# Kernel optimization log

Hardware: AMD Instinct MI355X
Metric: run time of the kernel (lower is better)

Reference implementation:

```python
import jax, jax.numpy as jnp
import numpy as np

N_NODES = 30000
N_EDGES = 600000
N_BATCH = 8
VFRAMES = 3
EPS = 1e-20


def rbf_func(D, num_rbf=16):
    # RBF over [0, 20] with num_rbf centers, matching torch rbf_func
    mu = jnp.linspace(0.0, 20.0, num_rbf).astype(D.dtype)
    sigma = 20.0 / num_rbf
    return jnp.exp(-(((D[..., None] - mu) / sigma) ** 2))


def decouple(U):
    # split vector into unit direction (zeroed when tiny) + RBF of its norm -> last dim 3+16
    sq = jnp.sum(U * U, axis=-1, keepdims=True)
    norm = jnp.sqrt(sq + 1e-12)  # tiny eps for grad safety; fwd diff negligible
    direct = jnp.where(norm < 1e-4, 0.0, U / (norm + 1e-6))
    return jnp.concatenate([direct, rbf_func(norm[..., 0])], axis=-1)


def int_embedding(d, num_embeddings):
    freq = jnp.exp(jnp.arange(0, num_embeddings, 2, dtype=jnp.float32) * (-np.log(10000.0) / num_embeddings))
    ang = d.astype(jnp.float32)[:, None] * freq[None, :]
    return jnp.concatenate([jnp.cos(ang), jnp.sin(ang)], axis=-1)


def make_frames(n_xyz, ca_xyz, c_xyz):
    # openfold Rigid.make_transform_from_reference -> R [N,3,3], t = CA [N,3]
    n = n_xyz - ca_xyz
    c = c_xyz - ca_xyz
    cx, cy, cz = c[:, 0], c[:, 1], c[:, 2]
    z = jnp.zeros_like(cx)
    o = jnp.ones_like(cx)
    nrm = jnp.sqrt(EPS + cx ** 2 + cy ** 2)
    s1, c1 = -cy / nrm, cx / nrm
    R1 = jnp.stack([c1, -s1, z, s1, c1, z, z, z, o], -1).reshape(-1, 3, 3)
    nrm2 = jnp.sqrt(EPS + cx ** 2 + cy ** 2 + cz ** 2)
    s2 = cz / nrm2
    c2 = jnp.sqrt(cx ** 2 + cy ** 2) / nrm2
    R2 = jnp.stack([c2, z, s2, z, o, z, -s2, z, c2], -1).reshape(-1, 3, 3)
    Rc = jnp.matmul(R2, R1)
    nrot = jnp.einsum('nij,nj->ni', Rc, n)
    ny, nz2 = nrot[:, 1], nrot[:, 2]
    nrm3 = jnp.sqrt(EPS + ny ** 2 + nz2 ** 2)
    sn, cn = -nz2 / nrm3, ny / nrm3
    Rn = jnp.stack([o, z, z, z, cn, -sn, z, sn, cn], -1).reshape(-1, 3, 3)
    R = jnp.swapaxes(jnp.matmul(Rn, Rc), -1, -2)
    return R, ca_xyz


def geo_features(X, node_idx, edge_idx, batch_id, num_batches, virtual_frame_num):
    N = X.shape[0]
    E = edge_idx.shape[1]
    B = num_batches          # static python int
    K = virtual_frame_num    # static python int
    src, dst = edge_idx[0], edge_idx[1]
    R, t = make_frames(X[:, 0], X[:, 1], X[:, 2])
    # relative transform T_ts = T[dst]^-1 . T[src]
    Rts = jnp.einsum('eji,ejk->eik', R[dst], R[src])            # [E,3,3]
    tts = jnp.einsum('eji,ej->ei', R[dst], t[src] - t[dst])     # [E,3]
    # node feats: consecutive-atom diffs, zeroed at each chain start, rotated into local frame
    flat = X.reshape(-1, 3)
    d = jnp.concatenate([jnp.zeros((1, 3), X.dtype), flat[1:] - flat[:-1]], 0).reshape(N, 4, 3)
    counts = jax.ops.segment_sum(jnp.ones_like(batch_id), batch_id, num_segments=B)
    shift = jnp.roll(jnp.cumsum(counts).at[-1].set(0), 1)       # chain start offsets
    d = d.at[shift].set(0.0)
    dX_loc = jnp.einsum('nji,naj->nai', R, d)                   # R^T @ d
    V = jnp.nan_to_num(decouple(dX_loc).reshape(N, -1))         # [N,76]
    # edge feats: both endpoints' atoms in src local frame
    pts = jnp.concatenate([X[src], X[dst]], axis=1)             # [E,8,3]
    loc = jnp.einsum('eji,eaj->eai', R[src], pts - t[src][:, None])
    diffE = decouple(loc).reshape(E, -1)                        # [E,152]
    pos = int_embedding((src - dst), 16)                        # [E,16]
    E_quant = jnp.swapaxes(Rts, -1, -2).reshape(E, 9)           # inverse rel-rot flattened
    E_trans = decouple(tts).reshape(E, -1)                      # [E,19]
    b = (node_idx[src] - node_idx[dst]).astype(X.dtype)
    E_bias = decouple(b[:, None, None]).reshape(E, -1)          # [E,17]
    Efeat = jnp.concatenate([diffE, E_quant, E_trans, pos, E_bias], axis=-1)  # [E,213]
    # virtual (global) frames: K virtual nodes per protein, identity frames (geo_frame=False)
    g_src = jnp.concatenate([N + batch_id + k * B for k in range(K)])   # [K*N]
    g_dst = jnp.tile(jnp.arange(N, dtype=batch_id.dtype), K)
    eidx_g = jnp.concatenate([jnp.stack([g_src, g_dst]), jnp.stack([g_dst, g_src])], axis=1)
    bid_g = jnp.tile(jnp.arange(B, dtype=batch_id.dtype), K)            # [K*B]
    V_g = int_embedding(jnp.repeat(jnp.arange(K), B), V.shape[-1]).astype(X.dtype)
    E_g = jnp.zeros((2 * K * N, Efeat.shape[-1]), Efeat.dtype)
    eyeKB = jnp.broadcast_to(jnp.eye(3, dtype=X.dtype), (K * B, 3, 3))
    V_out = jnp.concatenate([V, V_g], 0)
    E_out = jnp.concatenate([Efeat, E_g], 0)
    T_rot = jnp.concatenate([R, eyeKB], 0)
    T_trans = jnp.concatenate([t, jnp.zeros((K * B, 3), X.dtype)], 0)
    Tts_rot = jnp.concatenate([Rts, jnp.broadcast_to(jnp.eye(3, dtype=X.dtype), (2 * K * N, 3, 3))], 0)
    Tts_trans = jnp.concatenate([tts, jnp.zeros((2 * K * N, 3), X.dtype)], 0)
    batch_out = jnp.concatenate([batch_id, bid_g])
    eidx_out = jnp.concatenate([edge_idx, eidx_g], axis=1)
    return V_out, E_out, T_rot, T_trans, Tts_rot, Tts_trans, batch_out, eidx_out


def setup_inputs():
    key = jax.random.key(0)
    k1, k2 = jax.random.split(key)
    X = jax.random.normal(k1, (N_NODES, 4, 3), dtype=jnp.float32) * 4.0
    edge_idx = jax.random.randint(k2, (2, N_EDGES), 0, N_NODES)
    per = N_NODES // N_BATCH
    batch_id = jnp.repeat(jnp.arange(N_BATCH), per)   # sorted, contiguous batches
    node_idx = jnp.tile(jnp.arange(per), N_BATCH)     # residue index within each chain
    chain_encoding = batch_id % 8
    return {"X": X, "node_idx": node_idx, "edge_idx": edge_idx, "batch_id": batch_id,
            "chain_encoding": chain_encoding, "num_batches": N_BATCH, "virtual_frame_num": VFRAMES}


def reference(X, node_idx, edge_idx, batch_id, chain_encoding, num_batches, virtual_frame_num):
    V, Eo, T_rot, T_trans, Tts_rot, Tts_trans, batch_out, eidx_out = geo_features(
        X, node_idx, edge_idx, batch_id, num_batches, virtual_frame_num)
    K, B = virtual_frame_num, num_batches
    chain_out = jnp.concatenate([chain_encoding,
                                 jnp.ones((K * B,), chain_encoding.dtype) + 1000])
    return (V, Eo, T_rot, T_trans, Tts_rot, Tts_trans, batch_out, eidx_out, chain_out)
```

## Files before the change

kernel.cpp:

```cpp
#include <hip/hip_runtime.h>

typedef unsigned int u32;
typedef float f32x4 __attribute__((ext_vector_type(4)));

#define N_NODES 30000
#define N_EDGES 600000
#define NBATCH  8
#define KVF     3
#define PER_B   3750
#define NV      30024
#define EV      780000

#define O_V      0ULL
#define O_E      2281824ULL
#define O_TROT   168421824ULL
#define O_TTRANS 168692040ULL
#define O_TTSROT 168782112ULL
#define O_TTSTR  175802112ULL
#define O_BATCH  178142112ULL
#define O_EIDX   178172136ULL
#define O_CHAIN  179732136ULL

#define TOTAL_BLOCKS 12500
#define NODE_BLOCKS  118
#define FILL_THREADS 769792ULL
#define F_VE   9585000ULL
#define F_ROT  (F_VE + 405000ULL)
#define F_TR   (F_ROT + 135000ULL)
#define F_END  (F_TR + 390000ULL)

__device__ __forceinline__ float2 fast_sincos(float ang) {
    double rev = (double)ang * 0.15915494309189535;
    rev -= rint(rev);
    float r = (float)rev;
    float2 sc;
    sc.x = __builtin_amdgcn_sinf(r);
    sc.y = __builtin_amdgcn_cosf(r);
    return sc;
}

__device__ __forceinline__ void decouple_store(float u0, float u1, float u2, float* dst) {
    float sq   = u0 * u0 + u1 * u1 + u2 * u2;
    float norm = sqrtf(sq + 1e-12f);
    float inv  = (norm < 1e-4f) ? 0.f : (1.f / (norm + 1e-6f));
    dst[0] = u0 * inv;
    dst[1] = u1 * inv;
    dst[2] = u2 * inv;
#pragma unroll
    for (int k = 0; k < 16; ++k) {
        float mu = 1.3333333333333333f * (float)k;
        float z  = (norm - mu) * 0.8f;
        dst[3 + k] = __expf(-z * z);
    }
}

__device__ __forceinline__ void make_frame(float4 x0, float4 x1, float4 x2,
                                           float M[9], float& t0, float& t1, float& t2) {
    float cax = x0.w, cay = x1.x, caz = x1.y;
    float nx = x0.x - cax, ny = x0.y - cay, nz = x0.z - caz;
    float cx = x1.z - cax, cy = x1.w - cay, cz = x2.x - caz;
    float h2   = cx * cx + cy * cy;
    float nrm  = sqrtf(1e-20f + h2);
    float s1 = -cy / nrm, c1 = cx / nrm;
    float nrm2 = sqrtf(1e-20f + h2 + cz * cz);
    float s2 = cz / nrm2, c2 = sqrtf(h2) / nrm2;
    float Rc00 = c2 * c1, Rc01 = -c2 * s1, Rc02 = s2;
    float Rc10 = s1,      Rc11 = c1;
    float Rc20 = -s2 * c1, Rc21 = s2 * s1, Rc22 = c2;
    float nr1 = Rc10 * nx + Rc11 * ny;
    float nr2 = Rc20 * nx + Rc21 * ny + Rc22 * nz;
    float nrm3 = sqrtf(1e-20f + nr1 * nr1 + nr2 * nr2);
    float sn = -nr2 / nrm3, cn = nr1 / nrm3;
    M[0] = Rc00;                   M[1] = Rc01;                   M[2] = Rc02;
    M[3] = cn * Rc10 - sn * Rc20;  M[4] = cn * Rc11 - sn * Rc21;  M[5] = -sn * Rc22;
    M[6] = sn * Rc10 + cn * Rc20;  M[7] = sn * Rc11 + cn * Rc21;  M[8] = cn * Rc22;
    t0 = cax; t1 = cay; t2 = caz;
}

__global__ __launch_bounds__(256) void mega_kernel(
        const float* __restrict__ X, const int* __restrict__ eidx,
        const int* __restrict__ node_idx, const int* __restrict__ batch_id,
        const int* __restrict__ chain, float* __restrict__ out) {
    __shared__ __align__(16) float sE[64 * 213];
    __shared__ __align__(16) float sRot[64 * 9];
    __shared__ __align__(16) float sTr[64 * 3];

    int bid = blockIdx.x;
    int tid = threadIdx.x;

    if ((bid & 3) == 3) {
        int oblk = bid >> 2;
        if (oblk < NODE_BLOCKS) {
            int i = oblk * 256 + tid;
            if (i >= NV) return;
            if (i < N_NODES) {
                const float4* xv = (const float4*)(X + (size_t)i * 12);
                float4 x0 = xv[0], x1 = xv[1], x2 = xv[2];
                float M[9], cax, cay, caz;
                make_frame(x0, x1, x2, M, cax, cay, caz);
                float* tr = out + O_TROT + (size_t)i * 9;
                tr[0] = M[0]; tr[1] = M[3]; tr[2] = M[6];
                tr[3] = M[1]; tr[4] = M[4]; tr[5] = M[7];
                tr[6] = M[2]; tr[7] = M[5]; tr[8] = M[8];
                float* tt = out + O_TTRANS + (size_t)i * 3;
                tt[0] = cax; tt[1] = cay; tt[2] = caz;
                const float* xi = X + (size_t)i * 12;
                float* vp = out + O_V + (size_t)i * 76;
                bool zero_d = (i % PER_B) == 0;
#pragma unroll
                for (int a = 0; a < 4; ++a) {
                    float d0, d1, d2;
                    if (zero_d) {
                        d0 = d1 = d2 = 0.f;
                    } else {
                        const float* pc = xi + a * 3;
                        d0 = pc[0] - pc[-3]; d1 = pc[1] - pc[-2]; d2 = pc[2] - pc[-1];
                    }
                    float u0 = M[0] * d0 + M[1] * d1 + M[2] * d2;
                    float u1 = M[3] * d0 + M[4] * d1 + M[5] * d2;
                    float u2 = M[6] * d0 + M[7] * d1 + M[8] * d2;
                    decouple_store(u0, u1, u2, vp + a * 19);
                }
                out[O_BATCH + i] = (float)batch_id[i];
                out[O_CHAIN + i] = (float)chain[i];
            } else {
                int r = i - N_NODES;
                float kv = (float)(r >> 3);
                float* vp = out + O_V + (size_t)i * 76;
#pragma unroll
                for (int j = 0; j < 38; ++j) {
                    float freq = __expf((float)(2 * j) * (-9.210340371976184f / 76.f));
                    float2 sc  = fast_sincos(kv * freq);
                    vp[j]      = sc.y;
                    vp[38 + j] = sc.x;
                }
                float* tr = out + O_TROT + (size_t)i * 9;
#pragma unroll
                for (int j = 0; j < 9; ++j) tr[j] = (j == 0 || j == 4 || j == 8) ? 1.f : 0.f;
                float* tt = out + O_TTRANS + (size_t)i * 3;
                tt[0] = 0.f; tt[1] = 0.f; tt[2] = 0.f;
                out[O_BATCH + i] = (float)(r & 7);
                out[O_CHAIN + i] = 1001.f;
            }
            return;
        }
        f32x4* oE   = (f32x4*)(out + O_E + 600000ULL * 213ULL);
        f32x4* oRot = (f32x4*)(out + O_TTSROT + 5400000ULL);
        f32x4* oTr  = (f32x4*)(out + O_TTSTR + 1800000ULL);
        f32x4* oEi  = (f32x4*)(out + O_EIDX);
        f32x4 zero; zero.x = zero.y = zero.z = zero.w = 0.f;
        for (size_t f = (size_t)(oblk - NODE_BLOCKS) * 256 + tid; f < F_END; f += FILL_THREADS) {
            if (f < F_VE) {
                __builtin_nontemporal_store(zero, oE + f);
            } else if (f < F_ROT) {
                size_t f2 = f - F_VE;
                u32 a = (u32)((f2 * 4ULL) % 9ULL);
                f32x4 w;
#pragma unroll
                for (int l = 0; l < 4; ++l) {
                    w[l] = (a == 0u || a == 4u || a == 8u) ? 1.f : 0.f;
                    a = (a == 8u) ? 0u : a + 1u;
                }
                __builtin_nontemporal_store(w, oRot + f2);
            } else if (f < F_TR) {
                __builtin_nontemporal_store(zero, oTr + (f - F_ROT));
            } else {
                size_t f4 = f - F_TR;
                int i0 = (int)(f4 * 4);
                f32x4 w;
#pragma unroll
                for (int l = 0; l < 4; ++l) {
                    int i = i0 + l;
                    int row = (i >= EV) ? 1 : 0;
                    int col = i - row * EV;
                    float v;
                    if (col < N_EDGES) {
                        v = (float)eidx[row * N_EDGES + col];
                    } else {
                        int j    = col - N_EDGES;
                        int half = j / 90000;
                        int jj   = j - half * 90000;
                        int k    = jj / N_NODES;
                        int node = jj - k * N_NODES;
                        v = (row == half) ? (float)(N_NODES + batch_id[node] + k * NBATCH)
                                          : (float)node;
                    }
                    w[l] = v;
                }
                __builtin_nontemporal_store(w, oEi + f4);
            }
        }
        return;
    }

    int eblk = (bid >> 2) * 3 + (bid & 3);
    int el   = tid & 63;
    int part = tid >> 6;
    int e = eblk * 64 + el;
    int src = eidx[e];
    int dst = eidx[N_EDGES + e];
    float* se = sE + el * 213;

    if (part <= 1) {
        const float4* xs = (const float4*)(X + (size_t)src * 12);
        float4 s0 = xs[0], s1 = xs[1], s2 = xs[2];
        float4 p0 = s0, p1 = s1, p2 = s2;
        if (part == 1) {
            const float4* xd = (const float4*)(X + (size_t)dst * 12);
            p0 = xd[0]; p1 = xd[1]; p2 = xd[2];
        }
        float M[9], ts0, ts1, ts2;
        make_frame(s0, s1, s2, M, ts0, ts1, ts2);
        float px[4] = { p0.x, p0.w, p1.z, p2.y };
        float py[4] = { p0.y, p1.x, p1.w, p2.z };
        float pz[4] = { p0.z, p1.y, p2.x, p2.w };
        float* base = se + (part == 0 ? 0 : 76);
#pragma unroll
        for (int a = 0; a < 4; ++a) {
            float q0 = px[a] - ts0, q1 = py[a] - ts1, q2 = pz[a] - ts2;
            float u0 = M[0] * q0 + M[1] * q1 + M[2] * q2;
            float u1 = M[3] * q0 + M[4] * q1 + M[5] * q2;
            float u2 = M[6] * q0 + M[7] * q1 + M[8] * q2;
            decouple_store(u0, u1, u2, base + a * 19);
        }
    } else if (part == 2) {
        const float4* xs = (const float4*)(X + (size_t)src * 12);
        const float4* xd = (const float4*)(X + (size_t)dst * 12);
        float4 s0 = xs[0], s1 = xs[1], s2 = xs[2];
        float4 d0 = xd[0], d1 = xd[1], d2 = xd[2];
        float Ms[9], ts0, ts1, ts2;
        float Md[9], td0, td1, td2;
        make_frame(s0, s1, s2, Ms, ts0, ts1, ts2);
        make_frame(d0, d1, d2, Md, td0, td1, td2);
        float* sr = sRot + el * 9;
#pragma unroll
        for (int ii = 0; ii < 3; ++ii) {
#pragma unroll
            for (int k = 0; k < 3; ++k) {
                float q = Md[3 * ii] * Ms[3 * k] + Md[3 * ii + 1] * Ms[3 * k + 1]
                        + Md[3 * ii + 2] * Ms[3 * k + 2];
                sr[ii * 3 + k] = q;
                se[152 + k * 3 + ii] = q;
            }
        }
        float dt0 = ts0 - td0, dt1 = ts1 - td1, dt2 = ts2 - td2;
        float t0 = Md[0] * dt0 + Md[1] * dt1 + Md[2] * dt2;
        float t1 = Md[3] * dt0 + Md[4] * dt1 + Md[5] * dt2;
        float t2 = Md[6] * dt0 + Md[7] * dt1 + Md[8] * dt2;
        float* st = sTr + el * 3;
        st[0] = t0; st[1] = t1; st[2] = t2;
        decouple_store(t0, t1, t2, se + 161);
    } else {
        float dd = (float)(src - dst);
#pragma unroll
        for (int j = 0; j < 8; ++j) {
            float freq = __expf((float)(2 * j) * (-9.210340371976184f / 16.f));
            float ang  = dd * freq;
            float2 sc  = fast_sincos(ang);
            se[180 + j] = sc.y;
            se[188 + j] = sc.x;
        }
        float b    = (float)(node_idx[src] - node_idx[dst]);
        float norm = sqrtf(b * b + 1e-12f);
        se[196] = (norm < 1e-4f) ? 0.f : (b / (norm + 1e-6f));
#pragma unroll
        for (int k = 0; k < 16; ++k) {
            float z = (norm - 1.3333333333333333f * (float)k) * 0.8f;
            se[197 + k] = __expf(-z * z);
        }
    }
    __syncthreads();
    const f32x4* s4 = (const f32x4*)sE;
    f32x4* dE = (f32x4*)(out + O_E) + (size_t)eblk * 3408;
    for (int i2 = tid; i2 < 3408; i2 += 256)
        __builtin_nontemporal_store(s4[i2], dE + i2);
    if (tid < 144)
        __builtin_nontemporal_store(((const f32x4*)sRot)[tid],
                                    (f32x4*)(out + O_TTSROT) + (size_t)eblk * 144 + tid);
    if (tid < 48)
        __builtin_nontemporal_store(((const f32x4*)sTr)[tid],
                                    (f32x4*)(out + O_TTSTR) + (size_t)eblk * 48 + tid);
}

extern "C" void kernel_launch(void* const* d_in, const int* in_sizes, int n_in,
                              void* d_out, int out_size, void* d_ws, size_t ws_size,
                              hipStream_t stream) {
    const float* X        = (const float*)d_in[0];
    const int* node_idx   = (const int*)d_in[1];
    const int* eidx       = (const int*)d_in[2];
    const int* batch_id   = (const int*)d_in[3];
    const int* chain      = (const int*)d_in[4];
    float* out = (float*)d_out;
    (void)d_ws; (void)ws_size;

    mega_kernel<<<TOTAL_BLOCKS, 256, 0, stream>>>(X, eidx, node_idx, batch_id, chain, out);
}
```

Baseline: 715.7 us.

## Halve edges per block and split edge work across seven 32-lane parts

Each edge block now handles 32 edges instead of 64. The per-edge work is spread over seven 32-thread parts instead of four 64-thread parts: atom projections are split two per thread, and the sinusoidal and RBF features get separate parts. This gives more blocks, less shared memory per block and better thread utilisation, aimed at reducing per-thread latency and raising occupancy. The interleave of node/fill blocks changes from 1-in-4 to 1-in-7, and the source frame is recomputed in more threads (wave 7 of 8 idle).

```diff
diff --git a/kernel.cpp b/kernel.cpp
--- a/kernel.cpp
+++ b/kernel.cpp
@@ -21,7 +21,7 @@
 #define O_EIDX   178172136ULL
 #define O_CHAIN  179732136ULL
 
-#define TOTAL_BLOCKS 12500
+#define TOTAL_BLOCKS 21875
 #define NODE_BLOCKS  118
 #define FILL_THREADS 769792ULL
 #define F_VE   9585000ULL
@@ -81,15 +81,16 @@
         const float* __restrict__ X, const int* __restrict__ eidx,
         const int* __restrict__ node_idx, const int* __restrict__ batch_id,
         const int* __restrict__ chain, float* __restrict__ out) {
-    __shared__ __align__(16) float sE[64 * 213];
-    __shared__ __align__(16) float sRot[64 * 9];
-    __shared__ __align__(16) float sTr[64 * 3];
+    __shared__ __align__(16) float sE[32 * 213];
+    __shared__ __align__(16) float sRot[32 * 9];
+    __shared__ __align__(16) float sTr[32 * 3];
 
     int bid = blockIdx.x;
     int tid = threadIdx.x;
-
-    if ((bid & 3) == 3) {
-        int oblk = bid >> 2;
+    int sel = bid % 7;
+
+    if (sel == 6) {
+        int oblk = bid / 7;
         if (oblk < NODE_BLOCKS) {
             int i = oblk * 256 + tid;
             if (i >= NV) return;
@@ -193,37 +194,48 @@
         return;
     }
 
-    int eblk = (bid >> 2) * 3 + (bid & 3);
-    int el   = tid & 63;
-    int part = tid >> 6;
-    int e = eblk * 64 + el;
+    int eblk = (bid / 7) * 6 + sel;
+    int el   = tid & 31;
+    int part = tid >> 5;
+    int e = eblk * 32 + el;
     int src = eidx[e];
     int dst = eidx[N_EDGES + e];
     float* se = sE + el * 213;
 
-    if (part <= 1) {
+    if (part < 4) {
         const float4* xs = (const float4*)(X + (size_t)src * 12);
         float4 s0 = xs[0], s1 = xs[1], s2 = xs[2];
         float4 p0 = s0, p1 = s1, p2 = s2;
-        if (part == 1) {
+        if (part >= 2) {
             const float4* xd = (const float4*)(X + (size_t)dst * 12);
             p0 = xd[0]; p1 = xd[1]; p2 = xd[2];
         }
         float M[9], ts0, ts1, ts2;
         make_frame(s0, s1, s2, M, ts0, ts1, ts2);
-        float px[4] = { p0.x, p0.w, p1.z, p2.y };
-        float py[4] = { p0.y, p1.x, p1.w, p2.z };
-        float pz[4] = { p0.z, p1.y, p2.x, p2.w };
-        float* base = se + (part == 0 ? 0 : 76);
-#pragma unroll
-        for (int a = 0; a < 4; ++a) {
-            float q0 = px[a] - ts0, q1 = py[a] - ts1, q2 = pz[a] - ts2;
+        float A0x, A0y, A0z, A1x, A1y, A1z;
+        if (part & 1) {
+            A0x = p1.z; A0y = p1.w; A0z = p2.x;
+            A1x = p2.y; A1y = p2.z; A1z = p2.w;
+        } else {
+            A0x = p0.x; A0y = p0.y; A0z = p0.z;
+            A1x = p0.w; A1y = p1.x; A1z = p1.y;
+        }
+        float* base = se + (part >= 2 ? 76 : 0) + (part & 1) * 38;
+        {
+            float q0 = A0x - ts0, q1 = A0y - ts1, q2 = A0z - ts2;
             float u0 = M[0] * q0 + M[1] * q1 + M[2] * q2;
             float u1 = M[3] * q0 + M[4] * q1 + M[5] * q2;
             float u2 = M[6] * q0 + M[7] * q1 + M[8] * q2;
-            decouple_store(u0, u1, u2, base + a * 19);
-        }
-    } else if (part == 2) {
+            decouple_store(u0, u1, u2, base);
+        }
+        {
+            float q0 = A1x - ts0, q1 = A1y - ts1, q2 = A1z - ts2;
+            float u0 = M[0] * q0 + M[1] * q1 + M[2] * q2;
+            float u1 = M[3] * q0 + M[4] * q1 + M[5] * q2;
+            float u2 = M[6] * q0 + M[7] * q1 + M[8] * q2;
+            decouple_store(u0, u1, u2, base + 19);
+        }
+    } else if (part == 4) {
         const float4* xs = (const float4*)(X + (size_t)src * 12);
         const float4* xd = (const float4*)(X + (size_t)dst * 12);
         float4 s0 = xs[0], s1 = xs[1], s2 = xs[2];
@@ -250,16 +262,16 @@
         float* st = sTr + el * 3;
         st[0] = t0; st[1] = t1; st[2] = t2;
         decouple_store(t0, t1, t2, se + 161);
-    } else {
+    } else if (part == 5) {
         float dd = (float)(src - dst);
 #pragma unroll
         for (int j = 0; j < 8; ++j) {
             float freq = __expf((float)(2 * j) * (-9.210340371976184f / 16.f));
-            float ang  = dd * freq;
-            float2 sc  = fast_sincos(ang);
+            float2 sc  = fast_sincos(dd * freq);
             se[180 + j] = sc.y;
             se[188 + j] = sc.x;
         }
+    } else if (part == 6) {
         float b    = (float)(node_idx[src] - node_idx[dst]);
         float norm = sqrtf(b * b + 1e-12f);
         se[196] = (norm < 1e-4f) ? 0.f : (b / (norm + 1e-6f));
@@ -271,15 +283,15 @@
     }
     __syncthreads();
     const f32x4* s4 = (const f32x4*)sE;
-    f32x4* dE = (f32x4*)(out + O_E) + (size_t)eblk * 3408;
-    for (int i2 = tid; i2 < 3408; i2 += 256)
+    f32x4* dE = (f32x4*)(out + O_E) + (size_t)eblk * 1704;
+    for (int i2 = tid; i2 < 1704; i2 += 256)
         __builtin_nontemporal_store(s4[i2], dE + i2);
-    if (tid < 144)
+    if (tid < 72)
         __builtin_nontemporal_store(((const f32x4*)sRot)[tid],
-                                    (f32x4*)(out + O_TTSROT) + (size_t)eblk * 144 + tid);
-    if (tid < 48)
+                                    (f32x4*)(out + O_TTSROT) + (size_t)eblk * 72 + tid);
+    if (tid < 24)
         __builtin_nontemporal_store(((const f32x4*)sTr)[tid],
-                                    (f32x4*)(out + O_TTSTR) + (size_t)eblk * 48 + tid);
+                                    (f32x4*)(out + O_TTSTR) + (size_t)eblk * 24 + tid);
 }
 
 extern "C" void kernel_launch(void* const* d_in, const int* in_sizes, int n_in,
```

After: 712.2 us. No clear change (-0.5%).
